# Performance work log

Measured on AMD Instinct MI355X. Metric: run time of the kernel, lower is better.

Reference implementation:

```python
import jax, jax.numpy as jnp
import numpy as np

B, N, H = 16, 1024, 4
CH = (64, 128, 256, 512)
KV = 960
EPS = 1e-5  # InstanceNorm2d default eps


def setup_inputs() -> dict:
    key = jax.random.key(0)
    ks = jax.random.split(key, 16)
    s = 0.02
    inp = {
        "emb1": jax.random.normal(ks[0], (B, N, CH[0]), jnp.float32),
        "emb2": jax.random.normal(ks[1], (B, N, CH[1]), jnp.float32),
        "emb3": jax.random.normal(ks[2], (B, N, CH[2]), jnp.float32),
        "emb4": jax.random.normal(ks[3], (B, N, CH[3]), jnp.float32),
        "emb_all": jax.random.normal(ks[4], (B, N, KV), jnp.float32),
        # per-head query weights (torch Linear weight layout [out, in])
        "Wq1": jax.random.normal(ks[5], (H, CH[0] // 4, CH[0] // 4), jnp.float32) * s,
        "Wq2": jax.random.normal(ks[6], (H, CH[1] // 4, CH[1] // 4), jnp.float32) * s,
        "Wq3": jax.random.normal(ks[7], (H, CH[2] // 4, CH[2] // 4), jnp.float32) * s,
        "Wq4": jax.random.normal(ks[8], (H, CH[3] // 4, CH[3] // 4), jnp.float32) * s,
        # NOTE: original forward only ever uses self.key[0] / self.value[0]
        "Wk": jax.random.normal(ks[9], (KV // 4, KV // 4), jnp.float32) * s,
        "Wv": jax.random.normal(ks[10], (KV // 4, KV // 4), jnp.float32) * s,
        "Wo1": jax.random.normal(ks[11], (CH[0], CH[0]), jnp.float32) * s,
        "Wo2": jax.random.normal(ks[12], (CH[1], CH[1]), jnp.float32) * s,
        "Wo3": jax.random.normal(ks[13], (CH[2], CH[2]), jnp.float32) * s,
        "Wo4": jax.random.normal(ks[14], (CH[3], CH[3]), jnp.float32) * s,
    }
    return inp


def _heads_from_all(x):
    # Reproduce the per-head channel regrouping of emb_all:
    # head h takes [16h:16(h+1)] of scale1, [32h:...] of scale2, etc. -> [B,H,N,240]
    b, n, _ = x.shape
    parts = [
        x[:, :, 0:64].reshape(b, n, H, 16),
        x[:, :, 64:192].reshape(b, n, H, 32),
        x[:, :, 192:448].reshape(b, n, H, 64),
        x[:, :, 448:960].reshape(b, n, H, 128),
    ]
    return jnp.concatenate(parts, axis=-1).transpose(0, 2, 1, 3)


def _scale_attn(emb, Wq, Wo, Kh, Vh):
    b, n, c = emb.shape
    d = c // H
    q = emb.reshape(b, n, H, d)
    # per-head linear (torch: x @ W.T): [B,H,N,d]
    Qh = jnp.einsum('bnhd,hed->bhne', q, Wq)
    # channel attention: Q^T K -> [B,H,d,240]
    scores = jnp.einsum('bhnd,bhnk->bhdk', Qh, Kh) / np.float32(np.sqrt(KV))
    # InstanceNorm2d over heads (per (b,h), normalize over last two dims, biased var)
    m = scores.mean(axis=(2, 3), keepdims=True)
    v = scores.var(axis=(2, 3), keepdims=True)
    probs = jax.nn.softmax((scores - m) / jnp.sqrt(v + EPS), axis=-1)
    # probs @ V^T -> [B,H,d,N]
    ctx = jnp.einsum('bhdk,bhnk->bhdn', probs, Vh)
    # permute(0,3,2,1) -> [B,N,d,H], flatten -> [B,N,c]
    ctx = ctx.transpose(0, 3, 2, 1).reshape(b, n, c)
    return jnp.einsum('bnc,ec->bne', ctx, Wo)


def reference(emb1, emb2, emb3, emb4, emb_all,
              Wq1, Wq2, Wq3, Wq4, Wk, Wv, Wo1, Wo2, Wo3, Wo4):
    heads = _heads_from_all(emb_all)  # [B,H,N,240]
    Kh = jnp.einsum('bhnd,ed->bhne', heads, Wk)
    Vh = jnp.einsum('bhnd,ed->bhne', heads, Wv)
    O1 = _scale_attn(emb1, Wq1, Wo1, Kh, Vh)
    O2 = _scale_attn(emb2, Wq2, Wo2, Kh, Vh)
    O3 = _scale_attn(emb3, Wq3, Wo3, Kh, Vh)
    O4 = _scale_attn(emb4, Wq4, Wo4, Kh, Vh)
    return (O1, O2, O3, O4)
```

## Files before the change

### kernel.cpp

```cpp
#include <hip/hip_runtime.h>
#include <hip/hip_bf16.h>
#include <math.h>

#define B_   16
#define N_   1024
#define H_   4
#define D240 240
#define SC_  57600

typedef unsigned short ushort;
typedef __attribute__((ext_vector_type(8))) short bf16x8;
typedef __attribute__((ext_vector_type(8))) unsigned short u16x8;
typedef __attribute__((ext_vector_type(4))) float f32x4;

__device__ __forceinline__ ushort f2b(float v) {
  __hip_bfloat16 h = __float2bfloat16(v);
  return *reinterpret_cast<ushort*>(&h);
}

__device__ __forceinline__ u16x8 cvt8(float4 a, float4 b) {
  u16x8 w;
  w[0] = f2b(a.x); w[1] = f2b(a.y); w[2] = f2b(a.z); w[3] = f2b(a.w);
  w[4] = f2b(b.x); w[5] = f2b(b.y); w[6] = f2b(b.z); w[7] = f2b(b.w);
  return w;
}

__device__ __forceinline__ void gload16(const void* g, void* s) {
  __builtin_amdgcn_global_load_lds((const __attribute__((address_space(1))) void*)g,
                                   (__attribute__((address_space(3))) void*)s, 16, 0, 0);
}

__device__ __forceinline__ const float* heads_src(const float* __restrict__ emb_all,
                                                  int b, int n, int h, int k) {
  int soff;
  if (k < 16)       soff = h * 16 + k;
  else if (k < 48)  soff = 64  + h * 32  + (k - 16);
  else if (k < 112) soff = 192 + h * 64  + (k - 48);
  else              soff = 448 + h * 128 + (k - 112);
  return emb_all + ((long)b * N_ + n) * 960 + soff;
}

__device__ __forceinline__ const float* emb_src(const float* __restrict__ e1,
                                                const float* __restrict__ e2,
                                                const float* __restrict__ e3,
                                                const float* __restrict__ e4,
                                                int b, int n, int h, int k, int* stride) {
  if (k < 16)  { *stride = 64;  return e1 + ((long)b * N_ + n) * 64  + h * 16  + k; }
  if (k < 48)  { *stride = 128; return e2 + ((long)b * N_ + n) * 128 + h * 32  + (k - 16); }
  if (k < 112) { *stride = 256; return e3 + ((long)b * N_ + n) * 256 + h * 64  + (k - 48); }
  *stride = 512; return e4 + ((long)b * N_ + n) * 512 + h * 128 + (k - 112);
}

__global__ __launch_bounds__(256) void conv_weights(
    const float* __restrict__ Wk, const float* __restrict__ Wv,
    const float* __restrict__ q1, const float* __restrict__ q2,
    const float* __restrict__ q3, const float* __restrict__ q4,
    const float* __restrict__ o1, const float* __restrict__ o2,
    const float* __restrict__ o3, const float* __restrict__ o4,
    ushort* __restrict__ wts) {
  long i = (long)blockIdx.x * 256 + threadIdx.x;
  if (i >= 716800) return;
  float v = 0.f;
  if (i < 122880) {
    const float* src = (i < 61440) ? Wk : Wv;
    long j = (i < 61440) ? i : i - 61440;
    int r = j / 256, k = j % 256;
    if (k < 240) v = src[(long)r * 240 + k];
  } else if (i < 368640) {
    long j = i - 122880;
    int h = j / 61440; int rem = j % 61440;
    int r = rem / 256, k = rem % 256;
    int s = r < 16 ? 0 : r < 48 ? 1 : r < 112 ? 2 : 3;
    const int dss[4] = {16, 32, 64, 128};
    const int qf[4]  = {0, 16, 48, 112};
    const float* qs[4] = {q1, q2, q3, q4};
    int d = dss[s], off = qf[s];
    if (k >= off && k < off + d)
      v = qs[s][((long)(h * d + (r - off))) * d + (k - off)];
  } else {
    long j = i - 368640;
    int s = j < 4096 ? 0 : j < 20480 ? 1 : j < 86016 ? 2 : 3;
    const long base[4] = {0, 4096, 20480, 86016};
    const int cs[4] = {64, 128, 256, 512};
    const float* os[4] = {o1, o2, o3, o4};
    long rem = j - base[s];
    int c = cs[s], d = c >> 2;
    int e = rem / c, kk = rem % c;
    v = os[s][(long)e * c + (kk % d) * 4 + kk / d];
  }
  wts[i] = f2b(v);
}

__device__ __forceinline__ void core_w_g(
    ushort* As, ushort* Bs,
    const ushort* __restrict__ Aw, long lda, int M,
    const float* __restrict__ emb_all,
    const float* __restrict__ e1, const float* __restrict__ e2,
    const float* __restrict__ e3, const float* __restrict__ e4,
    int gmode, int b, int h,
    ushort* __restrict__ C, long ldc, int m0, int n0, int K)
{
  const int tid = threadIdx.x;
  const int l = tid & 63, w = tid >> 6;
  const int wy = w >> 1, wx = w & 1;

  f32x4 acc[4][4];
  #pragma unroll
  for (int i = 0; i < 4; ++i)
    #pragma unroll
    for (int j = 0; j < 4; ++j) acc[i][j] = (f32x4)0.f;

  const int srow = tid >> 2;
  const int skc  = (tid & 3) * 8;
  int ra0 = m0 + srow;      ra0 = ra0 < M ? ra0 : M - 1;
  int ra1 = m0 + srow + 64; ra1 = ra1 < M ? ra1 : M - 1;
  const ushort* a0 = Aw + (long)ra0 * lda + skc;
  const ushort* a1 = Aw + (long)ra1 * lda + skc;
  ushort* lA0 = As + srow * 32 + skc;
  ushort* lA1 = As + (srow + 64) * 32 + skc;
  ushort* lB0 = Bs + srow * 32 + skc;
  ushort* lB1 = Bs + (srow + 64) * 32 + skc;
  const int nrow = n0 + srow;

  const ushort* arp = As + (wy * 64 + (l & 15)) * 32 + (l >> 4) * 8;
  const ushort* brp = Bs + (wx * 64 + (l & 15)) * 32 + (l >> 4) * 8;

  for (int k0 = 0; k0 < K; k0 += 32) {
    __syncthreads();
    gload16(a0 + k0, lA0);
    gload16(a1 + k0, lA1);
    const int k = k0 + skc;
    u16x8 w0, w1;
    if (k < 240) {
      const float* s0; int stride;
      if (gmode == 0) { stride = 960; s0 = heads_src(emb_all, b, nrow, h, k); }
      else            { s0 = emb_src(e1, e2, e3, e4, b, nrow, h, k, &stride); }
      const float* s1 = s0 + (long)64 * stride;
      float4 p0 = *(const float4*)s0, p1 = *(const float4*)(s0 + 4);
      float4 q0 = *(const float4*)s1, q1 = *(const float4*)(s1 + 4);
      w0 = cvt8(p0, p1); w1 = cvt8(q0, q1);
    } else {
      w0 = (u16x8)0; w1 = (u16x8)0;
    }
    *(u16x8*)lB0 = w0;
    *(u16x8*)lB1 = w1;
    __syncthreads();
    bf16x8 af[4], bfr[4];
    #pragma unroll
    for (int i = 0; i < 4; ++i) af[i]  = *(const bf16x8*)(arp + i * 512);
    #pragma unroll
    for (int j = 0; j < 4; ++j) bfr[j] = *(const bf16x8*)(brp + j * 512);
    #pragma unroll
    for (int i = 0; i < 4; ++i)
      #pragma unroll
      for (int j = 0; j < 4; ++j)
        acc[i][j] = __builtin_amdgcn_mfma_f32_16x16x32_bf16(af[i], bfr[j], acc[i][j], 0, 0, 0);
  }

  const int quad = l >> 4, lc = l & 15;
  #pragma unroll
  for (int i = 0; i < 4; ++i) {
    #pragma unroll
    for (int r = 0; r < 4; ++r) {
      int row = m0 + wy * 64 + i * 16 + quad * 4 + r;
      if (row >= M) continue;
      ushort* Cr = C + (long)row * ldc;
      #pragma unroll
      for (int j = 0; j < 4; ++j) {
        int col = n0 + wx * 64 + j * 16 + lc;
        Cr[col] = f2b(acc[i][j][r]);
      }
    }
  }
}

__device__ __forceinline__ void core_g_w(
    ushort* As, ushort* Bs,
    const float* __restrict__ emb_all, int b, int h,
    const ushort* __restrict__ Bw, long ldb, int Nn, int Npad,
    ushort* __restrict__ C, long ldc, int m0, int n0, int K)
{
  const int tid = threadIdx.x;
  const int l = tid & 63, w = tid >> 6;
  const int wy = w >> 1, wx = w & 1;

  f32x4 acc[4][4];
  #pragma unroll
  for (int i = 0; i < 4; ++i)
    #pragma unroll
    for (int j = 0; j < 4; ++j) acc[i][j] = (f32x4)0.f;

  const int srow = tid >> 2;
  const int skc  = (tid & 3) * 8;
  int rb0 = n0 + srow;      rb0 = rb0 < Nn ? rb0 : Nn - 1;
  int rb1 = n0 + srow + 64; rb1 = rb1 < Nn ? rb1 : Nn - 1;
  const ushort* b0 = Bw + (long)rb0 * ldb + skc;
  const ushort* b1 = Bw + (long)rb1 * ldb + skc;
  ushort* lA0 = As + srow * 32 + skc;
  ushort* lA1 = As + (srow + 64) * 32 + skc;
  ushort* lB0 = Bs + srow * 32 + skc;
  ushort* lB1 = Bs + (srow + 64) * 32 + skc;
  const int mrow = m0 + srow;

  const ushort* arp = As + (wy * 64 + (l & 15)) * 32 + (l >> 4) * 8;
  const ushort* brp = Bs + (wx * 64 + (l & 15)) * 32 + (l >> 4) * 8;

  for (int k0 = 0; k0 < K; k0 += 32) {
    __syncthreads();
    gload16(b0 + k0, lB0);
    gload16(b1 + k0, lB1);
    const int k = k0 + skc;
    u16x8 w0, w1;
    if (k < 240) {
      const float* s0 = heads_src(emb_all, b, mrow, h, k);
      const float* s1 = s0 + (long)64 * 960;
      float4 p0 = *(const float4*)s0, p1 = *(const float4*)(s0 + 4);
      float4 q0 = *(const float4*)s1, q1 = *(const float4*)(s1 + 4);
      w0 = cvt8(p0, p1); w1 = cvt8(q0, q1);
    } else {
      w0 = (u16x8)0; w1 = (u16x8)0;
    }
    *(u16x8*)lA0 = w0;
    *(u16x8*)lA1 = w1;
    __syncthreads();
    bf16x8 af[4], bfr[4];
    #pragma unroll
    for (int i = 0; i < 4; ++i) af[i]  = *(const bf16x8*)(arp + i * 512);
    #pragma unroll
    for (int j = 0; j < 4; ++j) bfr[j] = *(const bf16x8*)(brp + j * 512);
    #pragma unroll
    for (int i = 0; i < 4; ++i)
      #pragma unroll
      for (int j = 0; j < 4; ++j)
        acc[i][j] = __builtin_amdgcn_mfma_f32_16x16x32_bf16(af[i], bfr[j], acc[i][j], 0, 0, 0);
  }

  const int quad = l >> 4, lc = l & 15;
  #pragma unroll
  for (int i = 0; i < 4; ++i) {
    #pragma unroll
    for (int r = 0; r < 4; ++r) {
      int row = m0 + wy * 64 + i * 16 + quad * 4 + r;
      ushort* Cr = C + (long)row * ldc;
      #pragma unroll
      for (int j = 0; j < 4; ++j) {
        int col = n0 + wx * 64 + j * 16 + lc;
        if (col < Nn) Cr[col] = f2b(acc[i][j][r]);
        else if (col < Npad) Cr[col] = 0;
      }
    }
  }
}

__global__ __launch_bounds__(256) void mfma_proj(
    const float* __restrict__ emb_all,
    const float* __restrict__ e1, const float* __restrict__ e2,
    const float* __restrict__ e3, const float* __restrict__ e4,
    const ushort* __restrict__ Wk_b, const ushort* __restrict__ Wv_b,
    const ushort* __restrict__ Wq_bd,
    ushort* __restrict__ Kh_T, ushort* __restrict__ Vh, ushort* __restrict__ Q_T)
{
  __shared__ __align__(16) ushort As[128 * 32];
  __shared__ __align__(16) ushort Bs[128 * 32];
  const int bx = blockIdx.x;

  if (bx < 1024) {
    const int bh = bx >> 4, t = bx & 15;
    const int b = bh >> 2, h = bh & 3;
    core_w_g(As, Bs, Wk_b, 256, 240,
             emb_all, e1, e2, e3, e4, 0, b, h,
             Kh_T + (long)bh * 240 * 1024, 1024,
             (t >> 3) * 128, (t & 7) * 128, 256);
  } else if (bx < 2048) {
    const int local = bx - 1024;
    const int bh = local >> 4, t = local & 15;
    const int b = bh >> 2, h = bh & 3;
    core_g_w(As, Bs, emb_all, b, h,
             Wv_b, 256, 240, 256,
             Vh + (long)bh * 1024 * 256, 256,
             (t >> 1) * 128, (t & 1) * 128, 256);
  } else {
    const int local = bx - 2048;
    const int bh = local >> 4, t = local & 15;
    const int b = bh >> 2, h = bh & 3;
    core_w_g(As, Bs, Wq_bd + h * 61440, 256, 240,
             emb_all, e1, e2, e3, e4, 1, b, h,
             Q_T + (long)bh * 240 * 1024, 1024,
             (t >> 3) * 128, (t & 7) * 128, 256);
  }
}

__global__ __launch_bounds__(256) void mfma_abT(
    const ushort* __restrict__ A, long lda, long AsY, long AsZ,
    const ushort* __restrict__ Bm, long ldb, long BsY, long BsZ,
    void* __restrict__ Cv, long ldc, long CsY, long CsZ,
    int M, int Nn, int Npad, int K, float alpha, int c_bf16, int tilesN)
{
  A  += blockIdx.y * AsY + blockIdx.z * AsZ;
  Bm += blockIdx.y * BsY + blockIdx.z * BsZ;

  const int m0 = (blockIdx.x / tilesN) * 128;
  const int n0 = (blockIdx.x % tilesN) * 128;
  const int tid = threadIdx.x;
  const int l = tid & 63, w = tid >> 6;
  const int wy = w >> 1, wx = w & 1;

  __shared__ __align__(16) ushort As[128 * 32];
  __shared__ __align__(16) ushort Bs[128 * 32];

  f32x4 acc[4][4];
  #pragma unroll
  for (int i = 0; i < 4; ++i)
    #pragma unroll
    for (int j = 0; j < 4; ++j) acc[i][j] = (f32x4)0.f;

  const int srow = tid >> 2;
  const int skc  = (tid & 3) * 8;
  int ra0 = m0 + srow;      ra0 = ra0 < M  ? ra0 : M - 1;
  int ra1 = m0 + srow + 64; ra1 = ra1 < M  ? ra1 : M - 1;
  int rb0 = n0 + srow;      rb0 = rb0 < Nn ? rb0 : Nn - 1;
  int rb1 = n0 + srow + 64; rb1 = rb1 < Nn ? rb1 : Nn - 1;
  const ushort* a0 = A  + (long)ra0 * lda + skc;
  const ushort* a1 = A  + (long)ra1 * lda + skc;
  const ushort* b0 = Bm + (long)rb0 * ldb + skc;
  const ushort* b1 = Bm + (long)rb1 * ldb + skc;
  ushort* lA0 = As + srow * 32 + skc;
  ushort* lA1 = As + (srow + 64) * 32 + skc;
  ushort* lB0 = Bs + srow * 32 + skc;
  ushort* lB1 = Bs + (srow + 64) * 32 + skc;

  const ushort* arp = As + (wy * 64 + (l & 15)) * 32 + (l >> 4) * 8;
  const ushort* brp = Bs + (wx * 64 + (l & 15)) * 32 + (l >> 4) * 8;

  for (int k0 = 0; k0 < K; k0 += 32) {
    __syncthreads();
    gload16(a0 + k0, lA0);
    gload16(a1 + k0, lA1);
    gload16(b0 + k0, lB0);
    gload16(b1 + k0, lB1);
    __syncthreads();
    bf16x8 af[4], bfr[4];
    #pragma unroll
    for (int i = 0; i < 4; ++i) af[i]  = *(const bf16x8*)(arp + i * 512);
    #pragma unroll
    for (int j = 0; j < 4; ++j) bfr[j] = *(const bf16x8*)(brp + j * 512);
    #pragma unroll
    for (int i = 0; i < 4; ++i)
      #pragma unroll
      for (int j = 0; j < 4; ++j)
        acc[i][j] = __builtin_amdgcn_mfma_f32_16x16x32_bf16(af[i], bfr[j], acc[i][j], 0, 0, 0);
  }

  const int quad = l >> 4, lc = l & 15;
  if (c_bf16) {
    ushort* C = (ushort*)Cv + blockIdx.y * CsY + blockIdx.z * CsZ;
    #pragma unroll
    for (int i = 0; i < 4; ++i) {
      #pragma unroll
      for (int r = 0; r < 4; ++r) {
        int row = m0 + wy * 64 + i * 16 + quad * 4 + r;
        if (row >= M) continue;
        ushort* Cr = C + (long)row * ldc;
        #pragma unroll
        for (int j = 0; j < 4; ++j) {
          int col = n0 + wx * 64 + j * 16 + lc;
          if (col < Nn) Cr[col] = f2b(acc[i][j][r] * alpha);
          else if (col < Npad) Cr[col] = 0;
        }
      }
    }
  } else {
    float* C = (float*)Cv + blockIdx.y * CsY + blockIdx.z * CsZ;
    #pragma unroll
    for (int i = 0; i < 4; ++i) {
      #pragma unroll
      for (int r = 0; r < 4; ++r) {
        int row = m0 + wy * 64 + i * 16 + quad * 4 + r;
        if (row >= M) continue;
        float* Cr = C + (long)row * ldc;
        #pragma unroll
        for (int j = 0; j < 4; ++j) {
          int col = n0 + wx * 64 + j * 16 + lc;
          if (col < Nn) Cr[col] = acc[i][j][r] * alpha;
        }
      }
    }
  }
}

__global__ __launch_bounds__(256) void mfma_ctx(const ushort* __restrict__ V,
                                                const ushort* __restrict__ P,
                                                ushort* __restrict__ ctx2) {
  const int h = blockIdx.y, b = blockIdx.z;
  const ushort* A  = V + (((long)b * H_ + h) * 1024) * 256;
  const ushort* Bm = P + (((long)b * H_ + h) * 240) * 256;

  const int m0 = (blockIdx.x >> 1) * 128;
  const int n0 = (blockIdx.x & 1) * 128;
  const int tid = threadIdx.x;
  const int l = tid & 63, w = tid >> 6;
  const int wy = w >> 1, wx = w & 1;

  __shared__ __align__(16) ushort As[128 * 32];
  __shared__ __align__(16) ushort Bs[128 * 32];

  f32x4 acc[4][4];
  #pragma unroll
  for (int i = 0; i < 4; ++i)
    #pragma unroll
    for (int j = 0; j < 4; ++j) acc[i][j] = (f32x4)0.f;

  const int srow = tid >> 2;
  const int skc  = (tid & 3) * 8;
  int rb0 = n0 + srow;      rb0 = rb0 < 240 ? rb0 : 239;
  int rb1 = n0 + srow + 64; rb1 = rb1 < 240 ? rb1 : 239;
  const ushort* a0 = A  + (long)(m0 + srow) * 256 + skc;
  const ushort* a1 = A  + (long)(m0 + srow + 64) * 256 + skc;
  const ushort* b0 = Bm + (long)rb0 * 256 + skc;
  const ushort* b1 = Bm + (long)rb1 * 256 + skc;
  ushort* lA0 = As + srow * 32 + skc;
  ushort* lA1 = As + (srow + 64) * 32 + skc;
  ushort* lB0 = Bs + srow * 32 + skc;
  ushort* lB1 = Bs + (srow + 64) * 32 + skc;

  const ushort* arp = As + (wy * 64 + (l & 15)) * 32 + (l >> 4) * 8;
  const ushort* brp = Bs + (wx * 64 + (l & 15)) * 32 + (l >> 4) * 8;

  for (int k0 = 0; k0 < 256; k0 += 32) {
    __syncthreads();
    gload16(a0 + k0, lA0);
    gload16(a1 + k0, lA1);
    gload16(b0 + k0, lB0);
    gload16(b1 + k0, lB1);
    __syncthreads();
    bf16x8 af[4], bfr[4];
    #pragma unroll
    for (int i = 0; i < 4; ++i) af[i]  = *(const bf16x8*)(arp + i * 512);
    #pragma unroll
    for (int j = 0; j < 4; ++j) bfr[j] = *(const bf16x8*)(brp + j * 512);
    #pragma unroll
    for (int i = 0; i < 4; ++i)
      #pragma unroll
      for (int j = 0; j < 4; ++j)
        acc[i][j] = __builtin_amdgcn_mfma_f32_16x16x32_bf16(af[i], bfr[j], acc[i][j], 0, 0, 0);
  }

  const int quad = l >> 4, lc = l & 15;
  const int dss[4] = {16, 32, 64, 128};
  const int qf[4]  = {0, 16, 48, 112};
  const int cf[4]  = {0, 64, 192, 448};
  #pragma unroll
  for (int i = 0; i < 4; ++i) {
    #pragma unroll
    for (int r = 0; r < 4; ++r) {
      int row = m0 + wy * 64 + i * 16 + quad * 4 + r;
      ushort* Cr = ctx2 + ((long)b * N_ + row) * 960;
      #pragma unroll
      for (int j = 0; j < 4; ++j) {
        int col = n0 + wx * 64 + j * 16 + lc;
        if (col < 240) {
          int s = col < 16 ? 0 : col < 48 ? 1 : col < 112 ? 2 : 3;
          int chan = cf[s] + h * dss[s] + (col - qf[s]);
          Cr[chan] = f2b(acc[i][j][r]);
        }
      }
    }
  }
}

__global__ __launch_bounds__(256) void mfma_oproj(const ushort* __restrict__ ctx2,
                                                  const ushort* __restrict__ Wo_b,
                                                  float* __restrict__ out) {
  const int bx = blockIdx.x;
  int s = bx < 128 ? 0 : bx < 256 ? 1 : bx < 512 ? 2 : 3;
  const int sbase[4] = {0, 128, 256, 512};
  const int cs_[4]   = {64, 128, 256, 512};
  const int coff_[4] = {0, 64, 192, 448};
  const int wo_[4]   = {0, 4096, 20480, 86016};
  const long oo_[4]  = {0, 1048576, 3145728, 7340032};
  const int c = cs_[s];
  const int nt = (c + 127) >> 7;
  const int local = bx - sbase[s];
  const int m0 = (local / nt) * 128;
  const int n0 = (local % nt) * 128;

  const ushort* A  = ctx2 + coff_[s];
  const ushort* Bm = Wo_b + wo_[s];
  float* C = out + oo_[s];
  const int K = c, Nn = c;

  const int tid = threadIdx.x;
  const int l = tid & 63, w = tid >> 6;
  const int wy = w >> 1, wx = w & 1;

  __shared__ __align__(16) ushort As[128 * 32];
  __shared__ __align__(16) ushort Bs[128 * 32];

  f32x4 acc[4][4];
  #pragma unroll
  for (int i = 0; i < 4; ++i)
    #pragma unroll
    for (int j = 0; j < 4; ++j) acc[i][j] = (f32x4)0.f;

  const int srow = tid >> 2;
  const int skc  = (tid & 3) * 8;
  int rb0 = n0 + srow;      rb0 = rb0 < Nn ? rb0 : Nn - 1;
  int rb1 = n0 + srow + 64; rb1 = rb1 < Nn ? rb1 : Nn - 1;
  const ushort* a0 = A  + (long)(m0 + srow) * 960 + skc;
  const ushort* a1 = A  + (long)(m0 + srow + 64) * 960 + skc;
  const ushort* b0 = Bm + (long)rb0 * c + skc;
  const ushort* b1 = Bm + (long)rb1 * c + skc;
  ushort* lA0 = As + srow * 32 + skc;
  ushort* lA1 = As + (srow + 64) * 32 + skc;
  ushort* lB0 = Bs + srow * 32 + skc;
  ushort* lB1 = Bs + (srow + 64) * 32 + skc;

  const ushort* arp = As + (wy * 64 + (l & 15)) * 32 + (l >> 4) * 8;
  const ushort* brp = Bs + (wx * 64 + (l & 15)) * 32 + (l >> 4) * 8;

  for (int k0 = 0; k0 < K; k0 += 32) {
    __syncthreads();
    gload16(a0 + k0, lA0);
    gload16(a1 + k0, lA1);
    gload16(b0 + k0, lB0);
    gload16(b1 + k0, lB1);
    __syncthreads();
    bf16x8 af[4], bfr[4];
    #pragma unroll
    for (int i = 0; i < 4; ++i) af[i]  = *(const bf16x8*)(arp + i * 512);
    #pragma unroll
    for (int j = 0; j < 4; ++j) bfr[j] = *(const bf16x8*)(brp + j * 512);
    #pragma unroll
    for (int i = 0; i < 4; ++i)
      #pragma unroll
      for (int j = 0; j < 4; ++j)
        acc[i][j] = __builtin_amdgcn_mfma_f32_16x16x32_bf16(af[i], bfr[j], acc[i][j], 0, 0, 0);
  }

  const int quad = l >> 4, lc = l & 15;
  #pragma unroll
  for (int i = 0; i < 4; ++i) {
    #pragma unroll
    for (int r = 0; r < 4; ++r) {
      int row = m0 + wy * 64 + i * 16 + quad * 4 + r;
      float* Cr = C + (long)row * c;
      #pragma unroll
      for (int j = 0; j < 4; ++j) {
        int col = n0 + wx * 64 + j * 16 + lc;
        if (col < Nn) Cr[col] = acc[i][j][r];
      }
    }
  }
}

__global__ __launch_bounds__(256) void in_stats(const float* __restrict__ sc0,
                                                const float* __restrict__ sc1,
                                                float* __restrict__ stats) {
  const int doffs[4] = {0, 16, 48, 112};
  const int dss[4]   = {16, 32, 64, 128};
  const int bh = blockIdx.x, sidx = blockIdx.y;
  const long base = (long)bh * SC_ + doffs[sidx] * D240;
  const float4* A4 = (const float4*)(sc0 + base);
  const float4* B4 = (const float4*)(sc1 + base);
  const int n4 = dss[sidx] * 60;

  float s = 0.f, s2 = 0.f;
  for (int i = threadIdx.x; i < n4; i += 256) {
    float4 a = A4[i], b = B4[i];
    float x0 = a.x + b.x, x1 = a.y + b.y, x2 = a.z + b.z, x3 = a.w + b.w;
    s  += x0 + x1 + x2 + x3;
    s2 += x0 * x0 + x1 * x1 + x2 * x2 + x3 * x3;
  }
  #pragma unroll
  for (int o = 32; o > 0; o >>= 1) { s += __shfl_down(s, o); s2 += __shfl_down(s2, o); }

  __shared__ float wsum[4], wsum2[4];
  const int wave = threadIdx.x >> 6, lane = threadIdx.x & 63;
  if (lane == 0) { wsum[wave] = s; wsum2[wave] = s2; }
  __syncthreads();
  if (threadIdx.x == 0) {
    float n = (float)(n4 * 4);
    float ts = wsum[0] + wsum[1] + wsum[2] + wsum[3];
    float ts2 = wsum2[0] + wsum2[1] + wsum2[2] + wsum2[3];
    float mean = ts / n;
    float var = ts2 / n - mean * mean;
    stats[(bh * 4 + sidx) * 2]     = mean;
    stats[(bh * 4 + sidx) * 2 + 1] = rsqrtf(var + 1e-5f);
  }
}

__global__ __launch_bounds__(256) void sm_apply(const float* __restrict__ sc0,
                                                const float* __restrict__ sc1,
                                                const float* __restrict__ stats,
                                                ushort* __restrict__ P) {
  const int bh = blockIdx.y;
  const int row = blockIdx.x * 4 + (threadIdx.x >> 6);
  const int lane = threadIdx.x & 63;
  const int s = row < 16 ? 0 : row < 48 ? 1 : row < 112 ? 2 : 3;
  const float mean = stats[(bh * 4 + s) * 2];
  const float rstd = stats[(bh * 4 + s) * 2 + 1];
  const long base = (long)bh * SC_ + (long)row * D240;
  const float* r0 = sc0 + base;
  const float* r1 = sc1 + base;
  ushort* p = P + ((long)bh * D240 + row) * 256;

  float v[4];
  float mx = -1e30f;
  #pragma unroll
  for (int j = 0; j < 4; ++j) {
    int c = lane + j * 64;
    v[j] = (c < D240) ? (r0[c] + r1[c] - mean) * rstd : -1e30f;
    mx = fmaxf(mx, v[j]);
  }
  #pragma unroll
  for (int o = 32; o > 0; o >>= 1) mx = fmaxf(mx, __shfl_xor(mx, o));
  float sum = 0.f;
  #pragma unroll
  for (int j = 0; j < 4; ++j) {
    int c = lane + j * 64;
    v[j] = (c < D240) ? __expf(v[j] - mx) : 0.f;
    sum += v[j];
  }
  #pragma unroll
  for (int o = 32; o > 0; o >>= 1) sum += __shfl_xor(sum, o);
  float inv = 1.f / sum;
  #pragma unroll
  for (int j = 0; j < 4; ++j) {
    int c = lane + j * 64;
    p[c] = (c < D240) ? f2b(v[j] * inv) : (ushort)0;
  }
}

extern "C" void kernel_launch(void* const* d_in, const int* in_sizes, int n_in,
                              void* d_out, int out_size, void* d_ws, size_t ws_size,
                              hipStream_t stream) {
  const float* emb[4] = {(const float*)d_in[0], (const float*)d_in[1],
                         (const float*)d_in[2], (const float*)d_in[3]};
  const float* emb_all = (const float*)d_in[4];
  const float* Wq[4] = {(const float*)d_in[5], (const float*)d_in[6],
                        (const float*)d_in[7], (const float*)d_in[8]};
  const float* Wk = (const float*)d_in[9];
  const float* Wv = (const float*)d_in[10];
  const float* Wo[4] = {(const float*)d_in[11], (const float*)d_in[12],
                        (const float*)d_in[13], (const float*)d_in[14]};
  float* out = (float*)d_out;
  float* sc0 = (float*)d_out;
  float* sc1 = (float*)d_out + 64L * SC_;

  ushort* wsb     = (ushort*)d_ws;
  ushort* ctx2    = wsb;
  ushort* P_b     = wsb + 16777216;
  ushort* Q_T     = wsb + 33554432;
  ushort* Kh_T    = wsb + 49283072;
  ushort* Vh      = wsb + 65011712;
  ushort* wts     = wsb + 81788928;
  ushort* Wk_b  = wts;
  ushort* Wv_b  = wts + 61440;
  ushort* Wq_bd = wts + 122880;
  ushort* Wo_b  = wts + 368640;
  float*  stats = (float*)(wsb + 82505728);

  const float alpha_s = 1.0f / sqrtf(960.0f);

  conv_weights<<<dim3(2800), 256, 0, stream>>>(Wk, Wv, Wq[0], Wq[1], Wq[2], Wq[3],
                                               Wo[0], Wo[1], Wo[2], Wo[3], wts);

  mfma_proj<<<dim3(3072), 256, 0, stream>>>(emb_all, emb[0], emb[1], emb[2], emb[3],
                                            Wk_b, Wv_b, Wq_bd, Kh_T, Vh, Q_T);

  mfma_abT<<<dim3(4, 64, 2), 256, 0, stream>>>(
      Q_T, 1024, 240L * 1024, 512,
      Kh_T, 1024, 240L * 1024, 512,
      sc0, 240, (long)SC_, 64L * SC_,
      240, 240, 240, 512, alpha_s, 0, 2);

  in_stats<<<dim3(64, 4), 256, 0, stream>>>(sc0, sc1, stats);
  sm_apply<<<dim3(60, 64), 256, 0, stream>>>(sc0, sc1, stats, P_b);

  mfma_ctx<<<dim3(16, H_, B_), 256, 0, stream>>>(Vh, P_b, ctx2);

  mfma_oproj<<<dim3(1024), 256, 0, stream>>>(ctx2, Wo_b, out);
}
```

Baseline: 350.4 us.

## Fuse score GEMM, instance-norm stats and softmax into one kernel

Replaces the split-K score GEMM, which wrote fp32 partial scores into the output buffer, and the separate instance-norm statistics and softmax kernels with a single kernel. Each block handles one (scale, batch-head) pair, runs the full K=1024 reduction with MFMA, and computes the mean/variance and row softmax from registers with shuffle and shared-memory reductions before writing bf16 probabilities. This removes the fp32 score round trip through global memory and two kernel launches. In exchange each block always computes a 128-row tile, so the smaller scales waste MFMA work, and the grid drops to 256 larger blocks with a longer serial K loop.

```diff
diff --git a/kernel.cpp b/kernel.cpp
--- a/kernel.cpp
+++ b/kernel.cpp
@@ -6,7 +6,6 @@
 #define N_   1024
 #define H_   4
 #define D240 240
-#define SC_  57600
 
 typedef unsigned short ushort;
 typedef __attribute__((ext_vector_type(8))) short bf16x8;
@@ -290,23 +289,23 @@
   }
 }
 
-__global__ __launch_bounds__(256) void mfma_abT(
-    const ushort* __restrict__ A, long lda, long AsY, long AsZ,
-    const ushort* __restrict__ Bm, long ldb, long BsY, long BsZ,
-    void* __restrict__ Cv, long ldc, long CsY, long CsZ,
-    int M, int Nn, int Npad, int K, float alpha, int c_bf16, int tilesN)
-{
-  A  += blockIdx.y * AsY + blockIdx.z * AsZ;
-  Bm += blockIdx.y * BsY + blockIdx.z * BsZ;
-
-  const int m0 = (blockIdx.x / tilesN) * 128;
-  const int n0 = (blockIdx.x % tilesN) * 128;
+__global__ __launch_bounds__(512) void fused_sm(const ushort* __restrict__ Q_T,
+                                                const ushort* __restrict__ Kh_T,
+                                                ushort* __restrict__ P,
+                                                float alpha) {
+  const int sidx = blockIdx.x, bh = blockIdx.y;
+  const int dss[4]   = {16, 32, 64, 128};
+  const int doffs[4] = {0, 16, 48, 112};
+  const int ds = dss[sidx], doff = doffs[sidx];
+
   const int tid = threadIdx.x;
   const int l = tid & 63, w = tid >> 6;
-  const int wy = w >> 1, wx = w & 1;
+  const int wy = w >> 2, wx = w & 3;
 
   __shared__ __align__(16) ushort As[128 * 32];
-  __shared__ __align__(16) ushort Bs[128 * 32];
+  __shared__ __align__(16) ushort Bs[256 * 32];
+  __shared__ float red[2][2][64][4];
+  __shared__ float wred[2][8];
 
   f32x4 acc[4][4];
   #pragma unroll
@@ -316,26 +315,22 @@
 
   const int srow = tid >> 2;
   const int skc  = (tid & 3) * 8;
-  int ra0 = m0 + srow;      ra0 = ra0 < M  ? ra0 : M - 1;
-  int ra1 = m0 + srow + 64; ra1 = ra1 < M  ? ra1 : M - 1;
-  int rb0 = n0 + srow;      rb0 = rb0 < Nn ? rb0 : Nn - 1;
-  int rb1 = n0 + srow + 64; rb1 = rb1 < Nn ? rb1 : Nn - 1;
-  const ushort* a0 = A  + (long)ra0 * lda + skc;
-  const ushort* a1 = A  + (long)ra1 * lda + skc;
-  const ushort* b0 = Bm + (long)rb0 * ldb + skc;
-  const ushort* b1 = Bm + (long)rb1 * ldb + skc;
+  const long qbase = (long)bh * 240 * 1024;
+  int qa = doff + (srow < ds ? srow : ds - 1);
+  const ushort* a0 = Q_T + qbase + (long)qa * 1024 + skc;
+  int kb1 = (srow + 128) < 240 ? (srow + 128) : 239;
+  const ushort* b0 = Kh_T + qbase + (long)srow * 1024 + skc;
+  const ushort* b1 = Kh_T + qbase + (long)kb1 * 1024 + skc;
   ushort* lA0 = As + srow * 32 + skc;
-  ushort* lA1 = As + (srow + 64) * 32 + skc;
   ushort* lB0 = Bs + srow * 32 + skc;
-  ushort* lB1 = Bs + (srow + 64) * 32 + skc;
+  ushort* lB1 = Bs + (srow + 128) * 32 + skc;
 
   const ushort* arp = As + (wy * 64 + (l & 15)) * 32 + (l >> 4) * 8;
   const ushort* brp = Bs + (wx * 64 + (l & 15)) * 32 + (l >> 4) * 8;
 
-  for (int k0 = 0; k0 < K; k0 += 32) {
+  for (int k0 = 0; k0 < 1024; k0 += 32) {
     __syncthreads();
     gload16(a0 + k0, lA0);
-    gload16(a1 + k0, lA1);
     gload16(b0 + k0, lB0);
     gload16(b1 + k0, lB1);
     __syncthreads();
@@ -352,37 +347,119 @@
   }
 
   const int quad = l >> 4, lc = l & 15;
-  if (c_bf16) {
-    ushort* C = (ushort*)Cv + blockIdx.y * CsY + blockIdx.z * CsZ;
-    #pragma unroll
-    for (int i = 0; i < 4; ++i) {
+
+  float s1 = 0.f, s2 = 0.f;
+  #pragma unroll
+  for (int i = 0; i < 4; ++i) {
+    #pragma unroll
+    for (int j = 0; j < 4; ++j) {
+      const int col = wx * 64 + j * 16 + lc;
       #pragma unroll
       for (int r = 0; r < 4; ++r) {
-        int row = m0 + wy * 64 + i * 16 + quad * 4 + r;
-        if (row >= M) continue;
-        ushort* Cr = C + (long)row * ldc;
-        #pragma unroll
-        for (int j = 0; j < 4; ++j) {
-          int col = n0 + wx * 64 + j * 16 + lc;
-          if (col < Nn) Cr[col] = f2b(acc[i][j][r] * alpha);
-          else if (col < Npad) Cr[col] = 0;
-        }
-      }
-    }
-  } else {
-    float* C = (float*)Cv + blockIdx.y * CsY + blockIdx.z * CsZ;
-    #pragma unroll
-    for (int i = 0; i < 4; ++i) {
-      #pragma unroll
-      for (int r = 0; r < 4; ++r) {
-        int row = m0 + wy * 64 + i * 16 + quad * 4 + r;
-        if (row >= M) continue;
-        float* Cr = C + (long)row * ldc;
-        #pragma unroll
-        for (int j = 0; j < 4; ++j) {
-          int col = n0 + wx * 64 + j * 16 + lc;
-          if (col < Nn) Cr[col] = acc[i][j][r] * alpha;
-        }
+        const int rl = wy * 64 + i * 16 + quad * 4 + r;
+        float v = acc[i][j][r] * alpha;
+        acc[i][j][r] = v;
+        if (rl < ds && col < 240) { s1 += v; s2 += v * v; }
+      }
+    }
+  }
+  #pragma unroll
+  for (int o = 32; o > 0; o >>= 1) { s1 += __shfl_xor(s1, o); s2 += __shfl_xor(s2, o); }
+  if (l == 0) { wred[0][w] = s1; wred[1][w] = s2; }
+  __syncthreads();
+  float ts = 0.f, ts2 = 0.f;
+  #pragma unroll
+  for (int ww = 0; ww < 8; ++ww) { ts += wred[0][ww]; ts2 += wred[1][ww]; }
+  const float cnt = (float)(ds * 240);
+  const float mean = ts / cnt;
+  const float var = ts2 / cnt - mean * mean;
+  const float rstd = rsqrtf(var + 1e-5f);
+
+  float rmax[4][4];
+  #pragma unroll
+  for (int i = 0; i < 4; ++i) {
+    #pragma unroll
+    for (int r = 0; r < 4; ++r) {
+      float m = -1e30f;
+      #pragma unroll
+      for (int j = 0; j < 4; ++j) {
+        const int col = wx * 64 + j * 16 + lc;
+        float z = (acc[i][j][r] - mean) * rstd;
+        acc[i][j][r] = z;
+        if (col < 240) m = fmaxf(m, z);
+      }
+      m = fmaxf(m, __shfl_xor(m, 1));
+      m = fmaxf(m, __shfl_xor(m, 2));
+      m = fmaxf(m, __shfl_xor(m, 4));
+      m = fmaxf(m, __shfl_xor(m, 8));
+      rmax[i][r] = m;
+    }
+  }
+  if (lc == 0) {
+    #pragma unroll
+    for (int i = 0; i < 4; ++i)
+      #pragma unroll
+      for (int r = 0; r < 4; ++r)
+        red[0][wy][i * 16 + quad * 4 + r][wx] = rmax[i][r];
+  }
+  __syncthreads();
+  #pragma unroll
+  for (int i = 0; i < 4; ++i) {
+    #pragma unroll
+    for (int r = 0; r < 4; ++r) {
+      const int rl = i * 16 + quad * 4 + r;
+      float m = red[0][wy][rl][0];
+      m = fmaxf(m, red[0][wy][rl][1]);
+      m = fmaxf(m, red[0][wy][rl][2]);
+      m = fmaxf(m, red[0][wy][rl][3]);
+      rmax[i][r] = m;
+    }
+  }
+
+  float rsum[4][4];
+  #pragma unroll
+  for (int i = 0; i < 4; ++i) {
+    #pragma unroll
+    for (int r = 0; r < 4; ++r) {
+      float sacc = 0.f;
+      #pragma unroll
+      for (int j = 0; j < 4; ++j) {
+        const int col = wx * 64 + j * 16 + lc;
+        float e = (col < 240) ? __expf(acc[i][j][r] - rmax[i][r]) : 0.f;
+        acc[i][j][r] = e;
+        sacc += e;
+      }
+      sacc += __shfl_xor(sacc, 1);
+      sacc += __shfl_xor(sacc, 2);
+      sacc += __shfl_xor(sacc, 4);
+      sacc += __shfl_xor(sacc, 8);
+      rsum[i][r] = sacc;
+    }
+  }
+  if (lc == 0) {
+    #pragma unroll
+    for (int i = 0; i < 4; ++i)
+      #pragma unroll
+      for (int r = 0; r < 4; ++r)
+        red[1][wy][i * 16 + quad * 4 + r][wx] = rsum[i][r];
+  }
+  __syncthreads();
+
+  #pragma unroll
+  for (int i = 0; i < 4; ++i) {
+    #pragma unroll
+    for (int r = 0; r < 4; ++r) {
+      const int rl = wy * 64 + i * 16 + quad * 4 + r;
+      if (rl >= ds) continue;
+      const int rli = i * 16 + quad * 4 + r;
+      float tot = red[1][wy][rli][0] + red[1][wy][rli][1] +
+                  red[1][wy][rli][2] + red[1][wy][rli][3];
+      float inv = 1.f / tot;
+      ushort* Pr = P + ((long)bh * 240 + doff + rl) * 256;
+      #pragma unroll
+      for (int j = 0; j < 4; ++j) {
+        const int col = wx * 64 + j * 16 + lc;
+        Pr[col] = (col < 240) ? f2b(acc[i][j][r] * inv) : (ushort)0;
       }
     }
   }
@@ -553,84 +630,6 @@
   }
 }
 
-__global__ __launch_bounds__(256) void in_stats(const float* __restrict__ sc0,
-                                                const float* __restrict__ sc1,
-                                                float* __restrict__ stats) {
-  const int doffs[4] = {0, 16, 48, 112};
-  const int dss[4]   = {16, 32, 64, 128};
-  const int bh = blockIdx.x, sidx = blockIdx.y;
-  const long base = (long)bh * SC_ + doffs[sidx] * D240;
-  const float4* A4 = (const float4*)(sc0 + base);
-  const float4* B4 = (const float4*)(sc1 + base);
-  const int n4 = dss[sidx] * 60;
-
-  float s = 0.f, s2 = 0.f;
-  for (int i = threadIdx.x; i < n4; i += 256) {
-    float4 a = A4[i], b = B4[i];
-    float x0 = a.x + b.x, x1 = a.y + b.y, x2 = a.z + b.z, x3 = a.w + b.w;
-    s  += x0 + x1 + x2 + x3;
-    s2 += x0 * x0 + x1 * x1 + x2 * x2 + x3 * x3;
-  }
-  #pragma unroll
-  for (int o = 32; o > 0; o >>= 1) { s += __shfl_down(s, o); s2 += __shfl_down(s2, o); }
-
-  __shared__ float wsum[4], wsum2[4];
-  const int wave = threadIdx.x >> 6, lane = threadIdx.x & 63;
-  if (lane == 0) { wsum[wave] = s; wsum2[wave] = s2; }
-  __syncthreads();
-  if (threadIdx.x == 0) {
-    float n = (float)(n4 * 4);
-    float ts = wsum[0] + wsum[1] + wsum[2] + wsum[3];
-    float ts2 = wsum2[0] + wsum2[1] + wsum2[2] + wsum2[3];
-    float mean = ts / n;
-    float var = ts2 / n - mean * mean;
-    stats[(bh * 4 + sidx) * 2]     = mean;
-    stats[(bh * 4 + sidx) * 2 + 1] = rsqrtf(var + 1e-5f);
-  }
-}
-
-__global__ __launch_bounds__(256) void sm_apply(const float* __restrict__ sc0,
-                                                const float* __restrict__ sc1,
-                                                const float* __restrict__ stats,
-                                                ushort* __restrict__ P) {
-  const int bh = blockIdx.y;
-  const int row = blockIdx.x * 4 + (threadIdx.x >> 6);
-  const int lane = threadIdx.x & 63;
-  const int s = row < 16 ? 0 : row < 48 ? 1 : row < 112 ? 2 : 3;
-  const float mean = stats[(bh * 4 + s) * 2];
-  const float rstd = stats[(bh * 4 + s) * 2 + 1];
-  const long base = (long)bh * SC_ + (long)row * D240;
-  const float* r0 = sc0 + base;
-  const float* r1 = sc1 + base;
-  ushort* p = P + ((long)bh * D240 + row) * 256;
-
-  float v[4];
-  float mx = -1e30f;
-  #pragma unroll
-  for (int j = 0; j < 4; ++j) {
-    int c = lane + j * 64;
-    v[j] = (c < D240) ? (r0[c] + r1[c] - mean) * rstd : -1e30f;
-    mx = fmaxf(mx, v[j]);
-  }
-  #pragma unroll
-  for (int o = 32; o > 0; o >>= 1) mx = fmaxf(mx, __shfl_xor(mx, o));
-  float sum = 0.f;
-  #pragma unroll
-  for (int j = 0; j < 4; ++j) {
-    int c = lane + j * 64;
-    v[j] = (c < D240) ? __expf(v[j] - mx) : 0.f;
-    sum += v[j];
-  }
-  #pragma unroll
-  for (int o = 32; o > 0; o >>= 1) sum += __shfl_xor(sum, o);
-  float inv = 1.f / sum;
-  #pragma unroll
-  for (int j = 0; j < 4; ++j) {
-    int c = lane + j * 64;
-    p[c] = (c < D240) ? f2b(v[j] * inv) : (ushort)0;
-  }
-}
-
 extern "C" void kernel_launch(void* const* d_in, const int* in_sizes, int n_in,
                               void* d_out, int out_size, void* d_ws, size_t ws_size,
                               hipStream_t stream) {
@@ -644,8 +643,6 @@
   const float* Wo[4] = {(const float*)d_in[11], (const float*)d_in[12],
                         (const float*)d_in[13], (const float*)d_in[14]};
   float* out = (float*)d_out;
-  float* sc0 = (float*)d_out;
-  float* sc1 = (float*)d_out + 64L * SC_;
 
   ushort* wsb     = (ushort*)d_ws;
   ushort* ctx2    = wsb;
@@ -658,7 +655,6 @@
   ushort* Wv_b  = wts + 61440;
   ushort* Wq_bd = wts + 122880;
   ushort* Wo_b  = wts + 368640;
-  float*  stats = (float*)(wsb + 82505728);
 
   const float alpha_s = 1.0f / sqrtf(960.0f);
 
@@ -668,14 +664,7 @@
   mfma_proj<<<dim3(3072), 256, 0, stream>>>(emb_all, emb[0], emb[1], emb[2], emb[3],
                                             Wk_b, Wv_b, Wq_bd, Kh_T, Vh, Q_T);
 
-  mfma_abT<<<dim3(4, 64, 2), 256, 0, stream>>>(
-      Q_T, 1024, 240L * 1024, 512,
-      Kh_T, 1024, 240L * 1024, 512,
-      sc0, 240, (long)SC_, 64L * SC_,
-      240, 240, 240, 512, alpha_s, 0, 2);
-
-  in_stats<<<dim3(64, 4), 256, 0, stream>>>(sc0, sc1, stats);
-  sm_apply<<<dim3(60, 64), 256, 0, stream>>>(sc0, sc1, stats, P_b);
+  fused_sm<<<dim3(4, 64), 512, 0, stream>>>(Q_T, Kh_T, P_b, alpha_s);
 
   mfma_ctx<<<dim3(16, H_, B_), 256, 0, stream>>>(Vh, P_b, ctx2);
 
```

Result: no change. 345.8 us (-1.3%).
